# Optimization experiments

Hardware: AMD Instinct MI355X
Metric: run time of the kernel (lower is better)

Reference implementation:

```python
import jax, jax.numpy as jnp
import numpy as np

# EdMIPS quantizer constants for 2-bit
HWGQ_STEP = 0.538      # hwgq_steps[2]
GAUSS_STEP = 0.996     # gaussian_steps[2]
ABIT = 2
WBIT = 2
BN_EPS = 1e-3


def setup_inputs() -> dict:
    key = jax.random.key(0)
    k1, k2 = jax.random.split(key, 2)
    x = jax.random.normal(k1, (32, 128, 56, 56), jnp.float32)
    gamma = jnp.ones((128,), jnp.float32)
    beta = jnp.zeros((128,), jnp.float32)
    weight = jax.random.normal(k2, (128, 128, 3, 3), jnp.float32) * 0.05
    return {"x": x, "gamma": gamma, "beta": beta, "weight": weight}


def _hwgq(x):
    # HWGQ: clamp to [0, step*(2^abit - 1)], then round to uniform levels.
    lvls = float(2 ** ABIT - 1)
    thr = HWGQ_STEP * lvls
    y = jnp.clip(x, 0.0, thr)
    q = jnp.round(y / HWGQ_STEP) * HWGQ_STEP
    # straight-through estimator: forward = q, backward = d/dy (clip mask)
    return y + jax.lax.stop_gradient(q - y)


def _gauss_quantize(w):
    # step scaled by weight std (detached, torch uses .item()); mid-rise quantizer.
    step = GAUSS_STEP * jax.lax.stop_gradient(jnp.std(w))
    lvls = float(2 ** WBIT) / 2.0
    q = (jnp.round(w / step + 0.5) - 0.5) * step
    thr = (lvls - 0.5) * step
    q = jnp.clip(q, -thr, thr)
    # full straight-through: backward = identity
    return w + jax.lax.stop_gradient(q - w)


def reference(x, gamma, beta, weight):
    # BatchNorm2d (training-mode batch stats, biased variance, eps=0.001)
    mean = jnp.mean(x, axis=(0, 2, 3), keepdims=True)
    var = jnp.var(x, axis=(0, 2, 3), keepdims=True)
    xn = (x - mean) * jax.lax.rsqrt(var + BN_EPS)
    xn = xn * gamma[None, :, None, None] + beta[None, :, None, None]
    # quantized activations and weights, then plain conv (bias=False)
    a = _hwgq(xn)
    qw = _gauss_quantize(weight)
    out = jax.lax.conv_general_dilated(
        a, qw,
        window_strides=(1, 1),
        padding=((1, 1), (1, 1)),
        dimension_numbers=("NCHW", "OIHW", "NCHW"),
    )
    return out  # [32, 128, 56, 56]
```

## Files before the change

kernel.cpp:

```cpp
#include <hip/hip_runtime.h>

typedef int i32x4 __attribute__((ext_vector_type(4)));

#define C_IN 128
#define HW 56
#define PIX 3136
#define NPLANE 401408
#define PROWB 7424
#define APAD_NSTRIDE 430592

static __device__ __forceinline__ void gload_lds16(const void* g, void* l) {
  __builtin_amdgcn_global_load_lds((__attribute__((address_space(1))) unsigned int*)g,
                                   (__attribute__((address_space(3))) unsigned int*)l, 16, 0, 0);
}

__global__ __launch_bounds__(256) void stats_k(const float* __restrict__ x,
                                               const float* __restrict__ w,
                                               double* __restrict__ bnpart,
                                               double* __restrict__ wpart) {
  const int b = blockIdx.x, tid = threadIdx.x;
  double s = 0.0, s2 = 0.0;
  if (b < 1024) {
    const int c = b & 127, sl = b >> 7;
    for (int n = sl * 4; n < sl * 4 + 4; ++n) {
      const float4* p = (const float4*)(x + (size_t)(n * C_IN + c) * PIX);
      for (int i = tid; i < PIX / 4; i += 256) {
        float4 v = p[i];
        s  += (double)v.x + (double)v.y + (double)v.z + (double)v.w;
        s2 += (double)v.x * v.x + (double)v.y * v.y + (double)v.z * v.z + (double)v.w * v.w;
      }
    }
  } else {
    const int wb = b - 1024;
    const float4* p = (const float4*)w;
    for (int i = wb * 576 + tid; i < (wb + 1) * 576; i += 256) {
      float4 v = p[i];
      s  += (double)v.x + (double)v.y + (double)v.z + (double)v.w;
      s2 += (double)v.x * v.x + (double)v.y * v.y + (double)v.z * v.z + (double)v.w * v.w;
    }
  }
  __shared__ double red[8];
  const int lane = tid & 63, wv = tid >> 6;
  for (int off = 32; off; off >>= 1) { s += __shfl_down(s, off); s2 += __shfl_down(s2, off); }
  if (lane == 0) { red[wv * 2] = s; red[wv * 2 + 1] = s2; }
  __syncthreads();
  if (tid == 0) {
    double* dst = (b < 1024) ? (bnpart + ((b & 127) * 8 + (b >> 7)) * 2)
                             : (wpart + (b - 1024) * 2);
    dst[0] = red[0] + red[2] + red[4] + red[6];
    dst[1] = red[1] + red[3] + red[5] + red[7];
  }
}

__global__ __launch_bounds__(256) void quant_k(const float* __restrict__ x,
                                               const float* __restrict__ w,
                                               const float* __restrict__ gamma,
                                               const float* __restrict__ beta,
                                               const double* __restrict__ bnpart,
                                               const double* __restrict__ wpart,
                                               signed char* __restrict__ apad,
                                               signed char* __restrict__ wq,
                                               float* __restrict__ stepp) {
  const int tid = threadIdx.x;
  if (blockIdx.y == 32) {
    const int bx = blockIdx.x;
    __shared__ float steps;
    __shared__ __align__(16) signed char wl[3 * 1152];
    if (tid < 64) {
      double s = wpart[tid * 2], s2 = wpart[tid * 2 + 1];
      for (int off = 32; off; off >>= 1) { s += __shfl_down(s, off); s2 += __shfl_down(s2, off); }
      if (tid == 0) {
        const double mean = s / 147456.0;
        const double var = s2 / 147456.0 - mean * mean;
        steps = 0.996f * (float)sqrt(var);
        if (bx == 0) stepp[0] = steps;
      }
    }
    __syncthreads();
    const float step = steps;
    for (int i = tid; i < 3456; i += 256) {
      const int oi = i / 1152, rem = i - oi * 1152;
      const int oc = bx + oi * 58;
      if (oc < 128) {
        const int c = rem / 9, rs = rem - c * 9;
        const float v = w[(size_t)(oc * C_IN + c) * 9 + rs];
        float t = 2.f * rintf(v / step + 0.5f) - 1.f;
        t = fminf(fmaxf(t, -3.f), 3.f);
        wl[oi * 1152 + rs * 128 + c] = (signed char)(int)t;
      }
    }
    __syncthreads();
    for (int i = tid; i < 216; i += 256) {
      const int oi = i / 72, rem = i - oi * 72;
      const int oc = bx + oi * 58;
      if (oc < 128) {
        const int rs = rem >> 3, c16 = rem & 7;
        *(uint4*)(wq + rs * 16384 + oc * 128 + c16 * 16) =
            *(const uint4*)(wl + oi * 1152 + rs * 128 + c16 * 16);
      }
    }
    return;
  }
  const int hh = blockIdx.x;
  const int n = blockIdx.y;
  __shared__ float2 aff[128];
  __shared__ __align__(16) signed char lds[58 * 144];
  if (tid < 128) {
    double s = 0.0, s2 = 0.0;
    for (int i = 0; i < 8; ++i) { s += bnpart[(tid * 8 + i) * 2]; s2 += bnpart[(tid * 8 + i) * 2 + 1]; }
    const double mean = s / 100352.0;
    const double var = s2 / 100352.0 - mean * mean;
    const double inv = 1.0 / sqrt(var + 1e-3);
    aff[tid] = make_float2((float)((double)gamma[tid] * inv),
                           (float)((double)beta[tid] - mean * inv * (double)gamma[tid]));
  }
  uint4* lds4 = (uint4*)lds;
  for (int i = tid; i < 58 * 144 / 16; i += 256) lds4[i] = make_uint4(0, 0, 0, 0);
  __syncthreads();
  if (hh >= 1 && hh <= 56) {
    const float* xp = x + (size_t)n * NPLANE + (hh - 1) * HW;
    for (int i = tid; i < C_IN * HW; i += 256) {
      const int ww = i % HW, c = i / HW;
      const float v = xp[(size_t)c * PIX + ww];
      const float2 af = aff[c];
      const float xn = fmaf(v, af.x, af.y);
      const float y = fminf(fmaxf(xn, 0.f), 1.614f);
      lds[(ww + 1) * 144 + c] = (signed char)(int)rintf(y * (1.f / 0.538f));
    }
  }
  __syncthreads();
  signed char* dst = apad + (size_t)n * APAD_NSTRIDE;
  for (int i = tid; i < 58 * 8; i += 256) {
    const int col = i >> 3, c16 = i & 7;
    const int pp = hh * 58 + col;
    *(uint4*)(dst + (((size_t)pp * 128 + c16 * 16) ^ ((pp & 7) << 4))) = lds4[col * 9 + c16];
  }
}

__global__ __launch_bounds__(256, 3) void conv_k(const signed char* __restrict__ apad,
                                                 const signed char* __restrict__ wq,
                                                 const float* __restrict__ stepp,
                                                 float* __restrict__ out) {
  __shared__ __align__(16) signed char Al[45056];
  const int bid = blockIdx.x;
  const int vid = (bid & 7) * 56 + (bid >> 3);
  const int n = vid / 14;
  const int rg = vid - n * 14;
  const int tid = threadIdx.x;
  const int wv = tid >> 6, lane = tid & 63;
  const int lr = lane & 15, q4 = lane >> 4;
  const int kq = q4 * 16;
  const int ohalf = (wv & 1) * 64;
  const int phalf = (wv >> 1) * 112;

  {
    const signed char* gsrc = apad + (size_t)n * APAD_NSTRIDE + (size_t)(rg * 4) * PROWB;
    for (int i = wv; i < 44; i += 4)
      if (i < 43 || lane < 32)
        gload_lds16(gsrc + i * 1024 + lane * 16, Al + i * 1024);
  }

  int pbase[7];
#pragma unroll
  for (int pf = 0; pf < 7; ++pf) {
    const int po = phalf + pf * 16 + lr;
    pbase[pf] = (po / 56) * 58 + po % 56;
  }

  i32x4 acc[7][4];
#pragma unroll
  for (int i = 0; i < 7; ++i)
#pragma unroll
    for (int j = 0; j < 4; ++j) acc[i][j] = (i32x4){0, 0, 0, 0};

  __syncthreads();

  for (int rs = 0; rs < 9; ++rs) {
    const int r = rs / 3, s = rs - 3 * r;
    const int poff = r * 58 + s;
    const signed char* wrow = wq + rs * 16384;
#pragma unroll
    for (int k64 = 0; k64 < 2; ++k64) {
      const int kb = k64 * 64 + kq;
      i32x4 wf[4];
#pragma unroll
      for (int of = 0; of < 4; ++of)
        wf[of] = *(const i32x4*)(wrow + (ohalf + of * 16 + lr) * 128 + kb);
#pragma unroll
      for (int pf = 0; pf < 7; ++pf) {
        const int p = pbase[pf] + poff;
        const i32x4 bf = *(const i32x4*)(Al + ((p * 128 + kb) ^ ((p & 7) << 4)));
        acc[pf][0] = __builtin_amdgcn_mfma_i32_16x16x64_i8(wf[0], bf, acc[pf][0], 0, 0, 0);
        acc[pf][1] = __builtin_amdgcn_mfma_i32_16x16x64_i8(wf[1], bf, acc[pf][1], 0, 0, 0);
        acc[pf][2] = __builtin_amdgcn_mfma_i32_16x16x64_i8(wf[2], bf, acc[pf][2], 0, 0, 0);
        acc[pf][3] = __builtin_amdgcn_mfma_i32_16x16x64_i8(wf[3], bf, acc[pf][3], 0, 0, 0);
      }
    }
  }

  const float oscale = 0.269f * stepp[0];
  float* outn = out + (size_t)n * NPLANE + (size_t)rg * 224;
#pragma unroll
  for (int pf = 0; pf < 7; ++pf) {
    const int po = phalf + pf * 16 + lr;
    float* op = outn + po;
#pragma unroll
    for (int of = 0; of < 4; ++of) {
      const int oc = ohalf + of * 16 + q4 * 4;
#pragma unroll
      for (int q = 0; q < 4; ++q)
        op[(size_t)(oc + q) * PIX] = (float)acc[pf][of][q] * oscale;
    }
  }
}

extern "C" void kernel_launch(void* const* d_in, const int* in_sizes, int n_in,
                              void* d_out, int out_size, void* d_ws, size_t ws_size,
                              hipStream_t stream) {
  const float* x = (const float*)d_in[0];
  const float* gamma = (const float*)d_in[1];
  const float* beta = (const float*)d_in[2];
  const float* w = (const float*)d_in[3];
  float* out = (float*)d_out;
  char* ws = (char*)d_ws;

  double* bnpart = (double*)(ws);
  double* wpart = (double*)(ws + 16384);
  float* stepp = (float*)(ws + 17408);
  signed char* wq = (signed char*)(ws + 18432);
  signed char* apad = (signed char*)(ws + 196608);

  stats_k<<<1088, 256, 0, stream>>>(x, w, bnpart, wpart);
  quant_k<<<dim3(58, 33), 256, 0, stream>>>(x, w, gamma, beta, bnpart, wpart, apad, wq, stepp);
  conv_k<<<448, 256, 0, stream>>>(apad, wq, stepp, out);
}
```

Baseline: 59.81 us.

## Split conv output channels across blocks and preload all weights into registers

```diff
diff --git a/kernel.cpp b/kernel.cpp
--- a/kernel.cpp
+++ b/kernel.cpp
@@ -137,20 +137,22 @@
   }
 }
 
-__global__ __launch_bounds__(256, 3) void conv_k(const signed char* __restrict__ apad,
+__global__ __launch_bounds__(256, 2) void conv_k(const signed char* __restrict__ apad,
                                                  const signed char* __restrict__ wq,
                                                  const float* __restrict__ stepp,
                                                  float* __restrict__ out) {
   __shared__ __align__(16) signed char Al[45056];
   const int bid = blockIdx.x;
-  const int vid = (bid & 7) * 56 + (bid >> 3);
-  const int n = vid / 14;
-  const int rg = vid - n * 14;
+  const int vid = (bid & 7) * 112 + (bid >> 3);
+  const int n = vid / 28;
+  const int rem = vid - n * 28;
+  const int rg = rem >> 1;
+  const int oh = rem & 1;
   const int tid = threadIdx.x;
   const int wv = tid >> 6, lane = tid & 63;
   const int lr = lane & 15, q4 = lane >> 4;
   const int kq = q4 * 16;
-  const int ohalf = (wv & 1) * 64;
+  const int ocb = oh * 64 + (wv & 1) * 32;
   const int phalf = (wv >> 1) * 112;
 
   {
@@ -160,6 +162,18 @@
         gload_lds16(gsrc + i * 1024 + lane * 16, Al + i * 1024);
   }
 
+  i32x4 wreg[9][2][2];
+  {
+    const signed char* wb = wq + (ocb + lr) * 128 + kq;
+#pragma unroll
+    for (int rs = 0; rs < 9; ++rs)
+#pragma unroll
+      for (int k64 = 0; k64 < 2; ++k64)
+#pragma unroll
+        for (int of = 0; of < 2; ++of)
+          wreg[rs][k64][of] = *(const i32x4*)(wb + rs * 16384 + of * 2048 + k64 * 64);
+  }
+
   int pbase[7];
 #pragma unroll
   for (int pf = 0; pf < 7; ++pf) {
@@ -167,33 +181,27 @@
     pbase[pf] = (po / 56) * 58 + po % 56;
   }
 
-  i32x4 acc[7][4];
-#pragma unroll
-  for (int i = 0; i < 7; ++i)
-#pragma unroll
-    for (int j = 0; j < 4; ++j) acc[i][j] = (i32x4){0, 0, 0, 0};
-
-  __syncthreads();
-
+  i32x4 acc[7][2];
+#pragma unroll
+  for (int i = 0; i < 7; ++i) {
+    acc[i][0] = (i32x4){0, 0, 0, 0};
+    acc[i][1] = (i32x4){0, 0, 0, 0};
+  }
+
+  __syncthreads();
+
+#pragma unroll
   for (int rs = 0; rs < 9; ++rs) {
-    const int r = rs / 3, s = rs - 3 * r;
-    const int poff = r * 58 + s;
-    const signed char* wrow = wq + rs * 16384;
+    const int poff = (rs / 3) * 58 + (rs % 3);
 #pragma unroll
     for (int k64 = 0; k64 < 2; ++k64) {
       const int kb = k64 * 64 + kq;
-      i32x4 wf[4];
-#pragma unroll
-      for (int of = 0; of < 4; ++of)
-        wf[of] = *(const i32x4*)(wrow + (ohalf + of * 16 + lr) * 128 + kb);
 #pragma unroll
       for (int pf = 0; pf < 7; ++pf) {
-        const int p = pbase[pf] + poff;
-        const i32x4 bf = *(const i32x4*)(Al + ((p * 128 + kb) ^ ((p & 7) << 4)));
-        acc[pf][0] = __builtin_amdgcn_mfma_i32_16x16x64_i8(wf[0], bf, acc[pf][0], 0, 0, 0);
-        acc[pf][1] = __builtin_amdgcn_mfma_i32_16x16x64_i8(wf[1], bf, acc[pf][1], 0, 0, 0);
-        acc[pf][2] = __builtin_amdgcn_mfma_i32_16x16x64_i8(wf[2], bf, acc[pf][2], 0, 0, 0);
-        acc[pf][3] = __builtin_amdgcn_mfma_i32_16x16x64_i8(wf[3], bf, acc[pf][3], 0, 0, 0);
+        const int pp = pbase[pf] + poff;
+        const i32x4 bf = *(const i32x4*)(Al + ((pp * 128 + kb) ^ ((pp & 7) << 4)));
+        acc[pf][0] = __builtin_amdgcn_mfma_i32_16x16x64_i8(wreg[rs][k64][0], bf, acc[pf][0], 0, 0, 0);
+        acc[pf][1] = __builtin_amdgcn_mfma_i32_16x16x64_i8(wreg[rs][k64][1], bf, acc[pf][1], 0, 0, 0);
       }
     }
   }
@@ -205,8 +213,8 @@
     const int po = phalf + pf * 16 + lr;
     float* op = outn + po;
 #pragma unroll
-    for (int of = 0; of < 4; ++of) {
-      const int oc = ohalf + of * 16 + q4 * 4;
+    for (int of = 0; of < 2; ++of) {
+      const int oc = ocb + of * 16 + q4 * 4;
 #pragma unroll
       for (int q = 0; q < 4; ++q)
         op[(size_t)(oc + q) * PIX] = (float)acc[pf][of][q] * oscale;
@@ -232,5 +240,5 @@
 
   stats_k<<<1088, 256, 0, stream>>>(x, w, bnpart, wpart);
   quant_k<<<dim3(58, 33), 256, 0, stream>>>(x, w, gamma, beta, bnpart, wpart, apad, wq, stepp);
-  conv_k<<<448, 256, 0, stream>>>(apad, wq, stepp, out);
-}
+  conv_k<<<896, 256, 0, stream>>>(apad, wq, stepp, out);
+}
```

After: 60.69 us. No clear change (+1.5%).
